# Kernel optimization log

Hardware: AMD Instinct MI355X
Metric: run time of the kernel (lower is better)

The kernel has to match this reference:

```python
import jax, jax.numpy as jnp
import numpy as np

N_NODES = 100000
N_EDGES = 1600000


def _degree_norms(src, dst, n):
    ones = jnp.ones(src.shape[0], dtype=jnp.float32)
    deg_out = jax.ops.segment_sum(ones, src, num_segments=n)
    deg_in = jax.ops.segment_sum(ones, dst, num_segments=n)
    src_norm = jax.lax.rsqrt(jnp.maximum(deg_out, 1.0))
    dst_norm = jax.lax.rsqrt(jnp.maximum(deg_in, 1.0))
    return src_norm, dst_norm


def _graph_conv(x, W, b, src, dst, src_norm, dst_norm, n):
    # DGL GraphConv, norm='both': D_dst^{-1/2} A D_src^{-1/2} X W + b
    # Apply W first (same math, smaller messages).
    h = x @ W                                  # [N, out]
    m = (h * src_norm[:, None])[src]           # [E, out] gather
    agg = jax.ops.segment_sum(m, dst, num_segments=n)  # [N, out] scatter-add
    return agg * dst_norm[:, None] + b


def setup_inputs() -> dict:
    key = jax.random.key(0)
    ks = jax.random.split(key, 10)
    inp = {
        "x": jax.random.normal(ks[0], (N_NODES, 128), dtype=jnp.float32),
        "src": jax.random.randint(ks[1], (N_EDGES,), 0, N_NODES, dtype=jnp.int32),
        "dst": jax.random.randint(ks[2], (N_EDGES,), 0, N_NODES, dtype=jnp.int32),
        "W1": jax.random.normal(ks[3], (128, 64), dtype=jnp.float32) * 0.08,
        "b1": jnp.zeros((64,), dtype=jnp.float32),
        "W2": jax.random.normal(ks[4], (64, 64), dtype=jnp.float32) * 0.12,
        "b2": jnp.zeros((64,), dtype=jnp.float32),
        "W3": jax.random.normal(ks[5], (64, 64), dtype=jnp.float32) * 0.12,
        "b3": jnp.zeros((64,), dtype=jnp.float32),
        "W4": jax.random.normal(ks[6], (64, 64), dtype=jnp.float32) * 0.12,
        "b4": jnp.zeros((64,), dtype=jnp.float32),
        "Wres": jax.random.normal(ks[7], (128, 64), dtype=jnp.float32) * 0.08,
        "bres": jnp.zeros((64,), dtype=jnp.float32),
        "Wop": jax.random.normal(ks[8], (64, 16), dtype=jnp.float32) * 0.12,
        "bop": jnp.zeros((16,), dtype=jnp.float32),
    }
    return inp


def reference(x, src, dst, W1, b1, W2, b2, W3, b3, W4, b4, Wres, bres, Wop, bop):
    n = x.shape[0]
    src_norm, dst_norm = _degree_norms(src, dst, n)
    res = x @ Wres + bres
    out = jax.nn.relu(_graph_conv(x, W1, b1, src, dst, src_norm, dst_norm, n))
    out = jax.nn.relu(_graph_conv(out, W2, b2, src, dst, src_norm, dst_norm, n))
    out = jax.nn.relu(_graph_conv(out, W3, b3, src, dst, src_norm, dst_norm, n))
    out = _graph_conv(out, W4, b4, src, dst, src_norm, dst_norm, n)
    out = jax.nn.relu(out + res)
    return out @ Wop + bop
```

## Files before the change

### kernel.cpp

```cpp
#include <hip/hip_runtime.h>
#include <cstdint>
#include <cstddef>


#define SLOTS 64
#define BCAP 5120
#define ACHUNK 4096

__device__ __forceinline__ unsigned short f2bf(float f) {
  union { float f; unsigned u; } v; v.f = f;
  unsigned r = (v.u + 0x7fffu + ((v.u >> 16) & 1u)) >> 16;
  return (unsigned short)r;
}
__device__ __forceinline__ float bf2f(unsigned short h) {
  union { unsigned u; float f; } v; v.u = ((unsigned)h) << 16;
  return v.f;
}
__device__ __forceinline__ void bf2x2(unsigned u, float* lo, float* hi) {
  union { unsigned x; float f; } a, b;
  a.x = u << 16; b.x = u & 0xFFFF0000u;
  *lo = a.f; *hi = b.f;
}

__global__ __launch_bounds__(256) void bucket_kernel(
    const int* __restrict__ src, const int* __restrict__ dst,
    int* __restrict__ gcur_d, int* __restrict__ gcur_s,
    unsigned* __restrict__ dbuck, unsigned char* __restrict__ sbuck,
    int E, int nbuck) {
  __shared__ int s_src[ACHUNK];
  __shared__ int s_dst[ACHUNK];
  __shared__ int run_d[512];
  __shared__ int run_s[512];
  const int t = threadIdx.x;
  const int base = blockIdx.x * ACHUNK;
  int cnt = E - base;
  if (cnt > ACHUNK) cnt = ACHUNK;

  for (int i = t; i < cnt; i += 256) {
    s_src[i] = src[base + i];
    s_dst[i] = dst[base + i];
  }
  for (int i = t; i < nbuck; i += 256) { run_d[i] = 0; run_s[i] = 0; }
  __syncthreads();
  for (int i = t; i < cnt; i += 256) {
    atomicAdd(&run_d[s_dst[i] >> 8], 1);
    atomicAdd(&run_s[s_src[i] >> 8], 1);
  }
  __syncthreads();
  {
    const int iters = (nbuck + 255) >> 8;
    for (int it = 0; it < iters; ++it) {
      int i = it * 256 + t;
      int hd = 0, hs = 0;
      if (i < nbuck) { hd = run_d[i]; hs = run_s[i]; }
      __syncthreads();
      if (i < nbuck) {
        run_d[i] = hd ? atomicAdd(&gcur_d[i], hd) : 0;
        run_s[i] = hs ? atomicAdd(&gcur_s[i], hs) : 0;
      }
      __syncthreads();
    }
  }
  for (int i = t; i < cnt; i += 256) {
    int d = s_dst[i], s = s_src[i];
    int bd = d >> 8;
    int pd = atomicAdd(&run_d[bd], 1);
    if (pd < BCAP) dbuck[(size_t)bd * BCAP + pd] = ((unsigned)(d & 255) << 24) | (unsigned)s;
    int bs = s >> 8;
    int ps = atomicAdd(&run_s[bs], 1);
    if (ps < BCAP) sbuck[(size_t)bs * BCAP + ps] = (unsigned char)(s & 255);
  }
}

__global__ __launch_bounds__(256) void csr_kernel(
    const unsigned* __restrict__ dbuck, const int* __restrict__ gcur_d,
    int* __restrict__ col, int* __restrict__ cnt_arr,
    float* __restrict__ dnorm, int N) {
  __shared__ int cur[256];
  const int b = blockIdx.x;
  const int t = threadIdx.x;
  const int node0 = b << 8;
  cur[t] = 0;
  __syncthreads();
  int cnt = gcur_d[b];
  if (cnt > BCAP) cnt = BCAP;
  const unsigned* p = dbuck + (size_t)b * BCAP;
  for (int i = t; i < cnt; i += 256) {
    unsigned e = p[i];
    int nl = e >> 24;
    int s = (int)(e & 0x00FFFFFFu);
    int pos = atomicAdd(&cur[nl], 1);
    if (pos < SLOTS) col[(size_t)(node0 + nl) * SLOTS + pos] = s;
  }
  __syncthreads();
  int node = node0 + t;
  if (node < N) {
    int c = cur[t];
    cnt_arr[node] = c;
    float d = (float)(c < 1 ? 1 : c);
    dnorm[node] = rsqrtf(d);
  }
}

__global__ __launch_bounds__(256) void degout_kernel(
    const unsigned char* __restrict__ sbuck, const int* __restrict__ gcur_s,
    float* __restrict__ snorm, int N) {
  __shared__ int cur[256];
  const int b = blockIdx.x;
  const int t = threadIdx.x;
  cur[t] = 0;
  __syncthreads();
  int cnt = gcur_s[b];
  if (cnt > BCAP) cnt = BCAP;
  const unsigned char* p = sbuck + (size_t)b * BCAP;
  for (int i = t; i < cnt; i += 256) atomicAdd(&cur[p[i]], 1);
  __syncthreads();
  int node = (b << 8) + t;
  if (node < N) {
    int c = cur[t];
    snorm[node] = rsqrtf((float)(c < 1 ? 1 : c));
  }
}

#define GEMM_STEP(r, aval, wv)                   \
  acc[r][0] = fmaf((aval), (wv).x, acc[r][0]);   \
  acc[r][1] = fmaf((aval), (wv).y, acc[r][1]);   \
  acc[r][2] = fmaf((aval), (wv).z, acc[r][2]);   \
  acc[r][3] = fmaf((aval), (wv).w, acc[r][3]);

#define GEMM_INNER_LOOP                                        \
  for (int kc = 0; kc < 64; kc += 4) {                         \
    float4 a0 = *(const float4*)&in_lds[ty4 + 0][kc];          \
    float4 a1 = *(const float4*)&in_lds[ty4 + 1][kc];          \
    float4 a2 = *(const float4*)&in_lds[ty4 + 2][kc];          \
    float4 a3 = *(const float4*)&in_lds[ty4 + 3][kc];          \
    float4 w0 = *(const float4*)&w_lds[kc + 0][tx4];           \
    float4 w1 = *(const float4*)&w_lds[kc + 1][tx4];           \
    float4 w2 = *(const float4*)&w_lds[kc + 2][tx4];           \
    float4 w3 = *(const float4*)&w_lds[kc + 3][tx4];           \
    GEMM_STEP(0, a0.x, w0) GEMM_STEP(0, a0.y, w1) GEMM_STEP(0, a0.z, w2) GEMM_STEP(0, a0.w, w3) \
    GEMM_STEP(1, a1.x, w0) GEMM_STEP(1, a1.y, w1) GEMM_STEP(1, a1.z, w2) GEMM_STEP(1, a1.w, w3) \
    GEMM_STEP(2, a2.x, w0) GEMM_STEP(2, a2.y, w1) GEMM_STEP(2, a2.z, w2) GEMM_STEP(2, a2.w, w3) \
    GEMM_STEP(3, a3.x, w0) GEMM_STEP(3, a3.y, w1) GEMM_STEP(3, a3.z, w2) GEMM_STEP(3, a3.w, w3) \
  }

template <int K>
__global__ __launch_bounds__(256) void gemm_f32_kernel(
    const float* __restrict__ X, const float* __restrict__ W,
    const float* __restrict__ norm, unsigned short* __restrict__ out, int n) {
  __shared__ float in_lds[64][68];
  __shared__ float w_lds[64][64];
  const int t = threadIdx.x;
  const int tx4 = (t & 15) * 4;
  const int ty4 = (t >> 4) * 4;
  const int node0 = blockIdx.x * 64;
  const int srow = t >> 2;
  const int scol = (t & 3) * 16;

  float acc[4][4];
#pragma unroll
  for (int r = 0; r < 4; r++)
#pragma unroll
    for (int j = 0; j < 4; j++) acc[r][j] = 0.f;

  for (int kb = 0; kb < K; kb += 64) {
    {
      int gi = node0 + srow;
      float4 v0, v1, v2, v3;
      if (gi < n) {
        const float* s = X + (size_t)gi * K + kb + scol;
        v0 = *(const float4*)(s + 0);
        v1 = *(const float4*)(s + 4);
        v2 = *(const float4*)(s + 8);
        v3 = *(const float4*)(s + 12);
      } else {
        v0 = v1 = v2 = v3 = make_float4(0.f, 0.f, 0.f, 0.f);
      }
      *(float4*)&in_lds[srow][scol + 0]  = v0;
      *(float4*)&in_lds[srow][scol + 4]  = v1;
      *(float4*)&in_lds[srow][scol + 8]  = v2;
      *(float4*)&in_lds[srow][scol + 12] = v3;
    }
    {
      const float* s = W + (size_t)(kb + srow) * 64 + scol;
      float4 w0 = *(const float4*)(s + 0);
      float4 w1 = *(const float4*)(s + 4);
      float4 w2 = *(const float4*)(s + 8);
      float4 w3 = *(const float4*)(s + 12);
      *(float4*)&w_lds[srow][scol + 0]  = w0;
      *(float4*)&w_lds[srow][scol + 4]  = w1;
      *(float4*)&w_lds[srow][scol + 8]  = w2;
      *(float4*)&w_lds[srow][scol + 12] = w3;
    }
    __syncthreads();
    GEMM_INNER_LOOP
    __syncthreads();
  }

#pragma unroll
  for (int r = 0; r < 4; r++) {
    int gi = node0 + ty4 + r;
    if (gi >= n) continue;
    float s = norm[gi];
    ushort4 o;
    o.x = f2bf(acc[r][0] * s);
    o.y = f2bf(acc[r][1] * s);
    o.z = f2bf(acc[r][2] * s);
    o.w = f2bf(acc[r][3] * s);
    *(ushort4*)&out[(size_t)gi * 64 + tx4] = o;
  }
}

__global__ __launch_bounds__(256) void gemm_bf16_kernel(
    const unsigned short* __restrict__ X, const float* __restrict__ W,
    const float* __restrict__ norm, unsigned short* __restrict__ out, int n) {
  __shared__ float in_lds[64][68];
  __shared__ float w_lds[64][64];
  const int t = threadIdx.x;
  const int tx4 = (t & 15) * 4;
  const int ty4 = (t >> 4) * 4;
  const int node0 = blockIdx.x * 64;
  const int srow = t >> 2;
  const int scol = (t & 3) * 16;

  float acc[4][4];
#pragma unroll
  for (int r = 0; r < 4; r++)
#pragma unroll
    for (int j = 0; j < 4; j++) acc[r][j] = 0.f;

  {
    int gi = node0 + srow;
    float f[16];
    if (gi < n) {
      const unsigned short* s = X + (size_t)gi * 64 + scol;
      uint4 u0 = *(const uint4*)(s + 0);
      uint4 u1 = *(const uint4*)(s + 8);
      bf2x2(u0.x, &f[0], &f[1]);   bf2x2(u0.y, &f[2], &f[3]);
      bf2x2(u0.z, &f[4], &f[5]);   bf2x2(u0.w, &f[6], &f[7]);
      bf2x2(u1.x, &f[8], &f[9]);   bf2x2(u1.y, &f[10], &f[11]);
      bf2x2(u1.z, &f[12], &f[13]); bf2x2(u1.w, &f[14], &f[15]);
    } else {
#pragma unroll
      for (int j = 0; j < 16; j++) f[j] = 0.f;
    }
#pragma unroll
    for (int j = 0; j < 16; j += 4)
      *(float4*)&in_lds[srow][scol + j] = make_float4(f[j], f[j+1], f[j+2], f[j+3]);
  }
  {
    const float* s = W + (size_t)srow * 64 + scol;
    float4 w0 = *(const float4*)(s + 0);
    float4 w1 = *(const float4*)(s + 4);
    float4 w2 = *(const float4*)(s + 8);
    float4 w3 = *(const float4*)(s + 12);
    *(float4*)&w_lds[srow][scol + 0]  = w0;
    *(float4*)&w_lds[srow][scol + 4]  = w1;
    *(float4*)&w_lds[srow][scol + 8]  = w2;
    *(float4*)&w_lds[srow][scol + 12] = w3;
  }
  __syncthreads();
  GEMM_INNER_LOOP

#pragma unroll
  for (int r = 0; r < 4; r++) {
    int gi = node0 + ty4 + r;
    if (gi >= n) continue;
    float s = norm[gi];
    ushort4 o;
    o.x = f2bf(acc[r][0] * s);
    o.y = f2bf(acc[r][1] * s);
    o.z = f2bf(acc[r][2] * s);
    o.w = f2bf(acc[r][3] * s);
    *(ushort4*)&out[(size_t)gi * 64 + tx4] = o;
  }
}

__global__ __launch_bounds__(256) void agg_kernel(
    const unsigned short* __restrict__ H, const int* __restrict__ cnt_arr,
    const int* __restrict__ col, const float* __restrict__ dnorm,
    const float* __restrict__ bias, unsigned short* __restrict__ O,
    int n, int do_relu) {
  int lane = threadIdx.x & 63;
  int wave = (blockIdx.x * blockDim.x + threadIdx.x) >> 6;
  int nwaves = (gridDim.x * blockDim.x) >> 6;
  float bb = bias[lane];
  for (int v = wave; v < n; v += nwaves) {
    int cnt = cnt_arr[v];
    if (cnt > SLOTS) cnt = SLOTS;
    size_t base = (size_t)v * SLOTS;
    int cv = (lane < cnt) ? col[base + lane] : 0;
    float a0 = 0.f, a1 = 0.f, a2 = 0.f, a3 = 0.f;
    float a4 = 0.f, a5 = 0.f, a6 = 0.f, a7 = 0.f;
    int jj = 0;
    for (; jj + 8 <= cnt; jj += 8) {
      int c0 = __shfl(cv, jj + 0);
      int c1 = __shfl(cv, jj + 1);
      int c2 = __shfl(cv, jj + 2);
      int c3 = __shfl(cv, jj + 3);
      int c4 = __shfl(cv, jj + 4);
      int c5 = __shfl(cv, jj + 5);
      int c6 = __shfl(cv, jj + 6);
      int c7 = __shfl(cv, jj + 7);
      a0 += bf2f(H[(size_t)c0 * 64 + lane]);
      a1 += bf2f(H[(size_t)c1 * 64 + lane]);
      a2 += bf2f(H[(size_t)c2 * 64 + lane]);
      a3 += bf2f(H[(size_t)c3 * 64 + lane]);
      a4 += bf2f(H[(size_t)c4 * 64 + lane]);
      a5 += bf2f(H[(size_t)c5 * 64 + lane]);
      a6 += bf2f(H[(size_t)c6 * 64 + lane]);
      a7 += bf2f(H[(size_t)c7 * 64 + lane]);
    }
    for (; jj + 4 <= cnt; jj += 4) {
      int c0 = __shfl(cv, jj + 0);
      int c1 = __shfl(cv, jj + 1);
      int c2 = __shfl(cv, jj + 2);
      int c3 = __shfl(cv, jj + 3);
      a0 += bf2f(H[(size_t)c0 * 64 + lane]);
      a1 += bf2f(H[(size_t)c1 * 64 + lane]);
      a2 += bf2f(H[(size_t)c2 * 64 + lane]);
      a3 += bf2f(H[(size_t)c3 * 64 + lane]);
    }
    for (; jj < cnt; jj++) {
      int c = __shfl(cv, jj);
      a0 += bf2f(H[(size_t)c * 64 + lane]);
    }
    float val = (((a0 + a1) + (a2 + a3)) + ((a4 + a5) + (a6 + a7))) * dnorm[v] + bb;
    if (do_relu) val = fmaxf(val, 0.f);
    O[base + lane] = f2bf(val);
  }
}

__global__ __launch_bounds__(256) void final_kernel(
    const float* __restrict__ X, const float* __restrict__ Wres,
    const float* __restrict__ bres, const unsigned short* __restrict__ O4,
    const float* __restrict__ Wop, const float* __restrict__ bop,
    float* __restrict__ out, int n) {
  __shared__ float in_lds[64][68];
  __shared__ float w_lds[64][64];
  __shared__ float wop_lds[64][16];
  const int t = threadIdx.x;
  const int tx4 = (t & 15) * 4;
  const int ty4 = (t >> 4) * 4;
  const int node0 = blockIdx.x * 64;
  const int srow = t >> 2;
  const int scol = (t & 3) * 16;

  ((float4*)&wop_lds[0][0])[t] = ((const float4*)Wop)[t];

  float acc[4][4];
#pragma unroll
  for (int r = 0; r < 4; r++)
#pragma unroll
    for (int j = 0; j < 4; j++) acc[r][j] = 0.f;

  for (int kb = 0; kb < 128; kb += 64) {
    {
      int gi = node0 + srow;
      float4 v0, v1, v2, v3;
      if (gi < n) {
        const float* s = X + (size_t)gi * 128 + kb + scol;
        v0 = *(const float4*)(s + 0);
        v1 = *(const float4*)(s + 4);
        v2 = *(const float4*)(s + 8);
        v3 = *(const float4*)(s + 12);
      } else {
        v0 = v1 = v2 = v3 = make_float4(0.f, 0.f, 0.f, 0.f);
      }
      *(float4*)&in_lds[srow][scol + 0]  = v0;
      *(float4*)&in_lds[srow][scol + 4]  = v1;
      *(float4*)&in_lds[srow][scol + 8]  = v2;
      *(float4*)&in_lds[srow][scol + 12] = v3;
    }
    {
      const float* s = Wres + (size_t)(kb + srow) * 64 + scol;
      float4 w0 = *(const float4*)(s + 0);
      float4 w1 = *(const float4*)(s + 4);
      float4 w2 = *(const float4*)(s + 8);
      float4 w3 = *(const float4*)(s + 12);
      *(float4*)&w_lds[srow][scol + 0]  = w0;
      *(float4*)&w_lds[srow][scol + 4]  = w1;
      *(float4*)&w_lds[srow][scol + 8]  = w2;
      *(float4*)&w_lds[srow][scol + 12] = w3;
    }
    __syncthreads();
    GEMM_INNER_LOOP
    __syncthreads();
  }

#pragma unroll
  for (int r = 0; r < 4; r++) {
    int gi = node0 + ty4 + r;
    float4 o = make_float4(0.f, 0.f, 0.f, 0.f);
    if (gi < n) {
      ushort4 v = *(const ushort4*)&O4[(size_t)gi * 64 + tx4];
      o.x = fmaxf(acc[r][0] + bres[tx4 + 0] + bf2f(v.x), 0.f);
      o.y = fmaxf(acc[r][1] + bres[tx4 + 1] + bf2f(v.y), 0.f);
      o.z = fmaxf(acc[r][2] + bres[tx4 + 2] + bf2f(v.z), 0.f);
      o.w = fmaxf(acc[r][3] + bres[tx4 + 3] + bf2f(v.w), 0.f);
    }
    *(float4*)&in_lds[ty4 + r][tx4] = o;
  }
  __syncthreads();

  {
    int nn = t >> 2;
    int fg = t & 3;
    float4 a = ((const float4*)bop)[fg];
#pragma unroll 16
    for (int k = 0; k < 64; k++) {
      float tv = in_lds[nn][k];
      float4 w = *(const float4*)&wop_lds[k][fg * 4];
      a.x = fmaf(tv, w.x, a.x);
      a.y = fmaf(tv, w.y, a.y);
      a.z = fmaf(tv, w.z, a.z);
      a.w = fmaf(tv, w.w, a.w);
    }
    int node = node0 + nn;
    if (node < n) *(float4*)&out[(size_t)node * 16 + fg * 4] = a;
  }
}

extern "C" void kernel_launch(void* const* d_in, const int* in_sizes, int n_in,
                              void* d_out, int out_size, void* d_ws, size_t ws_size,
                              hipStream_t stream) {
  const float* x    = (const float*)d_in[0];
  const int*   src  = (const int*)d_in[1];
  const int*   dst  = (const int*)d_in[2];
  const float* W1   = (const float*)d_in[3];
  const float* b1   = (const float*)d_in[4];
  const float* W2   = (const float*)d_in[5];
  const float* b2   = (const float*)d_in[6];
  const float* W3   = (const float*)d_in[7];
  const float* b3   = (const float*)d_in[8];
  const float* W4   = (const float*)d_in[9];
  const float* b4   = (const float*)d_in[10];
  const float* Wres = (const float*)d_in[11];
  const float* bres = (const float*)d_in[12];
  const float* Wop  = (const float*)d_in[13];
  const float* bop  = (const float*)d_in[14];
  float* out = (float*)d_out;

  const int N = in_sizes[0] / 128;
  const int E = in_sizes[1];
  const int nbuck = (N + 255) >> 8;

  char* p = (char*)d_ws;
  auto alloc = [&](size_t b) {
    char* r = p;
    p += (b + 255) & ~(size_t)255;
    return r;
  };
  int*            gcur_d  = (int*)alloc((size_t)nbuck * 4);
  int*            gcur_s  = (int*)alloc((size_t)nbuck * 4);
  unsigned*       dbuck   = (unsigned*)alloc((size_t)nbuck * BCAP * 4);
  unsigned char*  sbuck   = (unsigned char*)alloc((size_t)nbuck * BCAP);
  int*            col     = (int*)alloc((size_t)N * SLOTS * 4);
  int*            cnt_arr = (int*)alloc((size_t)N * 4);
  float*          snorm   = (float*)alloc((size_t)N * 4);
  float*          dnorm   = (float*)alloc((size_t)N * 4);
  unsigned short* Hbuf    = (unsigned short*)alloc((size_t)N * 64 * 2);
  unsigned short* Obuf    = (unsigned short*)alloc((size_t)N * 64 * 2);

  hipMemsetAsync(gcur_d, 0, (size_t)nbuck * 4, stream);
  hipMemsetAsync(gcur_s, 0, (size_t)nbuck * 4, stream);

  int ga = (E + ACHUNK - 1) / ACHUNK;
  bucket_kernel<<<ga, 256, 0, stream>>>(src, dst, gcur_d, gcur_s, dbuck, sbuck, E, nbuck);
  csr_kernel<<<nbuck, 256, 0, stream>>>(dbuck, gcur_d, col, cnt_arr, dnorm, N);
  degout_kernel<<<nbuck, 256, 0, stream>>>(sbuck, gcur_s, snorm, N);

  int gb = (N + 63) / 64;
  gemm_f32_kernel<128><<<gb, 256, 0, stream>>>(x, W1, snorm, Hbuf, N);
  agg_kernel<<<2048, 256, 0, stream>>>(Hbuf, cnt_arr, col, dnorm, b1, Obuf, N, 1);
  gemm_bf16_kernel<<<gb, 256, 0, stream>>>(Obuf, W2, snorm, Hbuf, N);
  agg_kernel<<<2048, 256, 0, stream>>>(Hbuf, cnt_arr, col, dnorm, b2, Obuf, N, 1);
  gemm_bf16_kernel<<<gb, 256, 0, stream>>>(Obuf, W3, snorm, Hbuf, N);
  agg_kernel<<<2048, 256, 0, stream>>>(Hbuf, cnt_arr, col, dnorm, b3, Obuf, N, 1);
  gemm_bf16_kernel<<<gb, 256, 0, stream>>>(Obuf, W4, snorm, Hbuf, N);
  agg_kernel<<<2048, 256, 0, stream>>>(Hbuf, cnt_arr, col, dnorm, b4, Obuf, N, 0);
  final_kernel<<<gb, 256, 0, stream>>>(x, Wres, bres, Obuf, Wop, bop, out, N);
}
```

Measured before the change: 339.6 us.

## Vectorize aggregation: each wave gathers four neighbor rows at once with 8-byte loads

The aggregation kernel splits each 64-lane wave into four 16-lane groups. Each group loads a full 128-byte bf16 neighbor row as uint2 (four features per lane), so four neighbors are fetched per wave instruction instead of one. Partial sums are combined across groups with xor shuffles, and the first group writes the output with a vector store. ReLU becomes a template parameter. This cuts the number of gather instructions and should raise memory-level parallelism, at the cost of a cross-lane reduction per node and idle lanes on the store.

```diff
diff --git a/kernel.cpp b/kernel.cpp
--- a/kernel.cpp
+++ b/kernel.cpp
@@ -276,58 +276,71 @@
   }
 }
 
+#define UNPACK_ADD(u, A)                         \
+  { float f0, f1, f2, f3;                        \
+    bf2x2((u).x, &f0, &f1);                      \
+    bf2x2((u).y, &f2, &f3);                      \
+    A[0] += f0; A[1] += f1; A[2] += f2; A[3] += f3; }
+
+template <int RELU>
 __global__ __launch_bounds__(256) void agg_kernel(
     const unsigned short* __restrict__ H, const int* __restrict__ cnt_arr,
     const int* __restrict__ col, const float* __restrict__ dnorm,
     const float* __restrict__ bias, unsigned short* __restrict__ O,
-    int n, int do_relu) {
-  int lane = threadIdx.x & 63;
-  int wave = (blockIdx.x * blockDim.x + threadIdx.x) >> 6;
-  int nwaves = (gridDim.x * blockDim.x) >> 6;
-  float bb = bias[lane];
+    int n) {
+  const int lane = threadIdx.x & 63;
+  const int sub = lane >> 4;
+  const int fl  = lane & 15;
+  const int wave = (blockIdx.x * blockDim.x + threadIdx.x) >> 6;
+  const int nwaves = (gridDim.x * blockDim.x) >> 6;
+  const uint2* __restrict__ H2 = (const uint2*)H;
+  const float4 bb = ((const float4*)bias)[fl];
+
   for (int v = wave; v < n; v += nwaves) {
     int cnt = cnt_arr[v];
     if (cnt > SLOTS) cnt = SLOTS;
-    size_t base = (size_t)v * SLOTS;
+    const size_t base = (size_t)v * SLOTS;
     int cv = (lane < cnt) ? col[base + lane] : 0;
-    float a0 = 0.f, a1 = 0.f, a2 = 0.f, a3 = 0.f;
-    float a4 = 0.f, a5 = 0.f, a6 = 0.f, a7 = 0.f;
-    int jj = 0;
-    for (; jj + 8 <= cnt; jj += 8) {
-      int c0 = __shfl(cv, jj + 0);
-      int c1 = __shfl(cv, jj + 1);
-      int c2 = __shfl(cv, jj + 2);
-      int c3 = __shfl(cv, jj + 3);
-      int c4 = __shfl(cv, jj + 4);
-      int c5 = __shfl(cv, jj + 5);
-      int c6 = __shfl(cv, jj + 6);
-      int c7 = __shfl(cv, jj + 7);
-      a0 += bf2f(H[(size_t)c0 * 64 + lane]);
-      a1 += bf2f(H[(size_t)c1 * 64 + lane]);
-      a2 += bf2f(H[(size_t)c2 * 64 + lane]);
-      a3 += bf2f(H[(size_t)c3 * 64 + lane]);
-      a4 += bf2f(H[(size_t)c4 * 64 + lane]);
-      a5 += bf2f(H[(size_t)c5 * 64 + lane]);
-      a6 += bf2f(H[(size_t)c6 * 64 + lane]);
-      a7 += bf2f(H[(size_t)c7 * 64 + lane]);
-    }
-    for (; jj + 4 <= cnt; jj += 4) {
-      int c0 = __shfl(cv, jj + 0);
-      int c1 = __shfl(cv, jj + 1);
-      int c2 = __shfl(cv, jj + 2);
-      int c3 = __shfl(cv, jj + 3);
-      a0 += bf2f(H[(size_t)c0 * 64 + lane]);
-      a1 += bf2f(H[(size_t)c1 * 64 + lane]);
-      a2 += bf2f(H[(size_t)c2 * 64 + lane]);
-      a3 += bf2f(H[(size_t)c3 * 64 + lane]);
-    }
-    for (; jj < cnt; jj++) {
-      int c = __shfl(cv, jj);
-      a0 += bf2f(H[(size_t)c * 64 + lane]);
-    }
-    float val = (((a0 + a1) + (a2 + a3)) + ((a4 + a5) + (a6 + a7))) * dnorm[v] + bb;
-    if (do_relu) val = fmaxf(val, 0.f);
-    O[base + lane] = f2bf(val);
+    float accA[4] = {0.f, 0.f, 0.f, 0.f};
+    float accB[4] = {0.f, 0.f, 0.f, 0.f};
+    int j = 0;
+    for (; j + 8 <= cnt; j += 8) {
+      int c0 = __shfl(cv, j + sub);
+      int c1 = __shfl(cv, j + 4 + sub);
+      uint2 u0 = H2[(size_t)c0 * 16 + fl];
+      uint2 u1 = H2[(size_t)c1 * 16 + fl];
+      UNPACK_ADD(u0, accA)
+      UNPACK_ADD(u1, accB)
+    }
+    for (; j < cnt; j += 4) {
+      int e = j + sub;
+      int c = __shfl(cv, e);
+      if (e < cnt) {
+        uint2 u = H2[(size_t)c * 16 + fl];
+        UNPACK_ADD(u, accA)
+      }
+    }
+#pragma unroll
+    for (int i = 0; i < 4; i++) {
+      float a = accA[i] + accB[i];
+      a += __shfl_xor(a, 16);
+      a += __shfl_xor(a, 32);
+      accA[i] = a;
+    }
+    if (sub == 0) {
+      float d = dnorm[v];
+      float v0 = accA[0] * d + bb.x;
+      float v1 = accA[1] * d + bb.y;
+      float v2 = accA[2] * d + bb.z;
+      float v3 = accA[3] * d + bb.w;
+      if (RELU) {
+        v0 = fmaxf(v0, 0.f); v1 = fmaxf(v1, 0.f);
+        v2 = fmaxf(v2, 0.f); v3 = fmaxf(v3, 0.f);
+      }
+      ushort4 o;
+      o.x = f2bf(v0); o.y = f2bf(v1); o.z = f2bf(v2); o.w = f2bf(v3);
+      *(ushort4*)&O[base + 4 * fl] = o;
+    }
   }
 }
 
@@ -472,12 +485,12 @@
 
   int gb = (N + 63) / 64;
   gemm_f32_kernel<128><<<gb, 256, 0, stream>>>(x, W1, snorm, Hbuf, N);
-  agg_kernel<<<2048, 256, 0, stream>>>(Hbuf, cnt_arr, col, dnorm, b1, Obuf, N, 1);
+  agg_kernel<1><<<2048, 256, 0, stream>>>(Hbuf, cnt_arr, col, dnorm, b1, Obuf, N);
   gemm_bf16_kernel<<<gb, 256, 0, stream>>>(Obuf, W2, snorm, Hbuf, N);
-  agg_kernel<<<2048, 256, 0, stream>>>(Hbuf, cnt_arr, col, dnorm, b2, Obuf, N, 1);
+  agg_kernel<1><<<2048, 256, 0, stream>>>(Hbuf, cnt_arr, col, dnorm, b2, Obuf, N);
   gemm_bf16_kernel<<<gb, 256, 0, stream>>>(Obuf, W3, snorm, Hbuf, N);
-  agg_kernel<<<2048, 256, 0, stream>>>(Hbuf, cnt_arr, col, dnorm, b3, Obuf, N, 1);
+  agg_kernel<1><<<2048, 256, 0, stream>>>(Hbuf, cnt_arr, col, dnorm, b3, Obuf, N);
   gemm_bf16_kernel<<<gb, 256, 0, stream>>>(Obuf, W4, snorm, Hbuf, N);
-  agg_kernel<<<2048, 256, 0, stream>>>(Hbuf, cnt_arr, col, dnorm, b4, Obuf, N, 0);
+  agg_kernel<0><<<2048, 256, 0, stream>>>(Hbuf, cnt_arr, col, dnorm, b4, Obuf, N);
   final_kernel<<<gb, 256, 0, stream>>>(x, Wres, bres, Obuf, Wop, bop, out, N);
 }
```

Result: faster. 325.7 us (-4.1%).
